# Optimization experiments

Hardware: AMD Instinct MI355X
Metric: run time of the kernel (lower is better)

Reference implementation:

```python
import jax, jax.numpy as jnp
import numpy as np

B, N, E = 4, 20000, 320000          # batch, billboards, edges
F_NODE, F_AD = 16, 8                # raw feature dims
H, L, HEADS = 64, 2, 4              # hidden, message-passing layers, attn heads


def layer_norm(x, g, b, eps=1e-5):
    mu = x.mean(-1, keepdims=True)
    var = ((x - mu) ** 2).mean(-1, keepdims=True)
    return (x - mu) / jnp.sqrt(var + eps) * g + b


def setup_inputs() -> dict:
    key = jax.random.key(0)
    ks = jax.random.split(key, 16)
    s = lambda i, shape, sc: jax.random.normal(ks[i], shape, jnp.float32) * sc
    return {
        'graph_nodes': s(0, (B, N, F_NODE), 1.0),
        'current_ad': s(1, (B, F_AD), 1.0),
        'w_node': s(2, (F_NODE, H), 0.1), 'b_node': jnp.zeros((H,), jnp.float32),
        'msg_w': s(3, (L, 2 * H, H), 0.05), 'msg_b': jnp.zeros((L, H), jnp.float32),
        'upd_w': s(4, (L, 2 * H, H), 0.05), 'upd_b': jnp.zeros((L, H), jnp.float32),
        'w_ad': s(5, (F_AD, H), 0.1), 'b_ad': jnp.zeros((H,), jnp.float32),
        'wq': s(6, (H, H), 0.1), 'bq': jnp.zeros((H,), jnp.float32),
        'wk': s(7, (H, H), 0.1), 'bk': jnp.zeros((H,), jnp.float32),
        'wv': s(8, (H, H), 0.1), 'bv': jnp.zeros((H,), jnp.float32),
        'wo': s(9, (H, H), 0.1), 'bo': jnp.zeros((H,), jnp.float32),
        'ln_g': jnp.ones((H,), jnp.float32), 'ln_b': jnp.zeros((H,), jnp.float32),
        'policy_w': s(10, (H,), 0.1), 'policy_b': jnp.zeros((), jnp.float32),
        'graph_edge_links': jax.random.randint(ks[11], (B, 2, E), 0, N),
        'mask': jax.random.randint(ks[12], (B, N), 0, 2).astype(bool),
    }


def reference(graph_nodes, current_ad, w_node, b_node, msg_w, msg_b, upd_w, upd_b,
              w_ad, b_ad, wq, bq, wk, bk, wv, bv, wo, bo, ln_g, ln_b,
              policy_w, policy_b, graph_edge_links, mask):
    # ---- node encoder ----
    h = jax.nn.relu(graph_nodes @ w_node + b_node)          # [B,N,H]
    src = graph_edge_links[:, 0, :]                          # [B,E]
    dst = graph_edge_links[:, 1, :]                          # [B,E]
    gather = jax.vmap(lambda hh, ii: hh[ii])                 # per-batch edge gather
    scatter = jax.vmap(lambda m, d: jax.ops.segment_sum(m, d, num_segments=N))
    # ---- message passing: gather -> MLP message -> scatter-add -> residual update ----
    for l in range(L):
        edge_in = jnp.concatenate([gather(h, src), gather(h, dst)], axis=-1)  # [B,E,2H]
        msg = jax.nn.relu(edge_in @ msg_w[l] + msg_b[l])                       # [B,E,H]
        agg = scatter(msg, dst)                                                # [B,N,H]
        h = h + jax.nn.relu(jnp.concatenate([h, agg], axis=-1) @ upd_w[l] + upd_b[l])
    # ---- ad encoder + multi-head attention (query=ad, key/value=billboards) ----
    a = jax.nn.relu(current_ad @ w_ad + b_ad)                # [B,H]
    dh = H // HEADS
    q = (a @ wq + bq).reshape(B, HEADS, 1, dh)               # [B,h,1,d]
    k = (h @ wk + bk).reshape(B, N, HEADS, dh).transpose(0, 2, 1, 3)  # [B,h,N,d]
    v = (h @ wv + bv).reshape(B, N, HEADS, dh).transpose(0, 2, 1, 3)
    att = jax.nn.softmax(jnp.einsum('bhqd,bhkd->bhqk', q, k) / jnp.sqrt(jnp.float32(dh)), axis=-1)
    ctx = jnp.einsum('bhqk,bhkd->bhqd', att, v).reshape(B, H)
    g = layer_norm(a + ctx @ wo + bo, ln_g, ln_b)            # residual + LN, [B,H]
    # ---- masked policy logits over billboards ----
    logits = jnp.einsum('bnh,bh->bn', h, g) / jnp.sqrt(jnp.float32(H)) + h @ policy_w + policy_b
    return jnp.where(mask, logits, jnp.float32(-1e9))
```

## Files before the change

### kernel.cpp

```cpp
#include <hip/hip_runtime.h>
#include <hip/hip_bf16.h>
#include <math.h>

constexpr int B_ = 4;
constexpr int N_ = 20000;
constexpr int E_ = 320000;
constexpr int HEADS_ = 4;
constexpr int NCH = 64;
constexpr int CS = (N_ + NCH - 1) / NCH;
constexpr int NT_ = (B_ * N_) / 16;
constexpr int NWIN = 1250;
constexpr int HWIN = 625;
constexpr int WCAP = 512;
constexpr int TPAD = 16;

typedef __attribute__((ext_vector_type(8))) short short8;
typedef __attribute__((ext_vector_type(4))) float f32x4;

constexpr size_t SZ_TDB   = (size_t)B_ * N_ * 64 * 2;
constexpr size_t SZ_AGG   = (size_t)B_ * N_ * 64 * 4;
constexpr size_t SZ_EBUCK = (size_t)B_ * NWIN * WCAP * 4;
constexpr size_t SZ_EPAIR = (size_t)B_ * E_ * 4;
constexpr size_t OFF_TDB  = 0;
constexpr size_t OFF_AGG  = SZ_TDB;
constexpr size_t OFF_EBUCK= OFF_AGG + SZ_AGG;
constexpr size_t OFF_EPAIR= OFF_EBUCK + SZ_EBUCK;
constexpr size_t OFF_HB16 = OFF_EPAIR + SZ_EPAIR;
constexpr size_t OFF_AVEC = OFF_HB16 + SZ_TDB;
constexpr size_t OFF_Q    = OFF_AVEC + 1024;
constexpr size_t OFF_CTX  = OFF_Q + 1024;
constexpr size_t OFF_WCMB = OFF_CTX + 1024;
constexpr size_t OFF_FLAG = OFF_WCMB + 1024;
constexpr size_t OFF_PART = OFF_FLAG + 64;
constexpr size_t OFF_TAILS= OFF_PART + 1024 * 18 * 4 + 64;
constexpr size_t OFF_WBASE= OFF_TAILS + (size_t)B_ * NWIN * TPAD * 4;
constexpr size_t OFF_VB16 = OFF_WBASE + (size_t)B_ * NWIN * 4 + 64;

static __device__ __forceinline__ unsigned short f2bf(float f) {
    union { float f; unsigned u; } v; v.f = f;
    unsigned r = v.u + 0x7fffu + ((v.u >> 16) & 1u);
    return (unsigned short)(r >> 16);
}
static __device__ __forceinline__ float bf2f(unsigned short u) {
    union { unsigned u; float f; } v; v.u = (unsigned)u << 16;
    return v.f;
}

__global__ void k_maskdetect(const unsigned int* __restrict__ m, int* __restrict__ flag) {
    if (blockIdx.x == 0 && threadIdx.x == 0) {
        bool alli = true, allf = true;
        for (int i = 0; i < 256; ++i) {
            unsigned v = m[i];
            alli = alli && (v <= 1u);
            allf = allf && (v == 0u || v == 0x3f800000u);
        }
        *flag = alli ? 1 : (allf ? 2 : 0);
    }
}

__global__ __launch_bounds__(256) void k_embed_bucket(const float* __restrict__ gn,
                                                      const float* __restrict__ wnod,
                                                      const float* __restrict__ bias,
                                                      unsigned short* __restrict__ hb16,
                                                      const int* __restrict__ links,
                                                      int* __restrict__ tails,
                                                      unsigned* __restrict__ ebuck) {
    int i = blockIdx.x;
    int g = i >> 3, r = i & 7;
    if (g % 5 == 4) {
        int eb = (g / 5) * 8 + r;
        int lane = threadIdx.x & 63;
        float wc[16];
#pragma unroll
        for (int k = 0; k < 16; ++k) wc[k] = wnod[k * 64 + lane];
        float bb = bias[lane];
        int gw = eb * 4 + (threadIdx.x >> 6);
        for (int node = gw; node < B_ * N_; node += 1248 * 4) {
            const float* rr = gn + (size_t)node * 16;
            float a0 = 0.f, a1 = 0.f, a2 = 0.f, a3 = 0.f;
#pragma unroll
            for (int k = 0; k < 16; k += 4) {
                a0 = fmaf(rr[k + 0], wc[k + 0], a0);
                a1 = fmaf(rr[k + 1], wc[k + 1], a1);
                a2 = fmaf(rr[k + 2], wc[k + 2], a2);
                a3 = fmaf(rr[k + 3], wc[k + 3], a3);
            }
            float v = fmaxf(bb + ((a0 + a1) + (a2 + a3)), 0.f);
            hb16[(size_t)node * 64 + lane] = f2bf(v);
        }
    } else {
        int og = g - (g + 1) / 5;
        int b = r >> 1;
        int half = r & 1;
        int e0 = og * 512 + threadIdx.x;
        const int* lsrc = links + (size_t)b * 2 * E_;
#pragma unroll
        for (int ch = 0; ch < 2; ++ch) {
            int e = e0 + ch * 256;
            unsigned src = (unsigned)lsrc[e];
            unsigned dst = (unsigned)lsrc[E_ + e];
            int w = dst >> 4;
            if ((w >= HWIN) == (half == 1)) {
                int slot = atomicAdd(&tails[(b * NWIN + w) * TPAD], 1);
                if (slot < WCAP)
                    ebuck[(size_t)(b * NWIN + w) * WCAP + slot] = (dst << 16) | src;
            }
        }
    }
}

__global__ __launch_bounds__(1024) void k_scan_tails(const int* __restrict__ tails,
                                                     int* __restrict__ wbase) {
    __shared__ int wsum[16];
    __shared__ int sbase;
    int b = blockIdx.x, t = threadIdx.x;
    int lane = t & 63, wv = t >> 6;
    if (t == 0) sbase = 0;
    __syncthreads();
    for (int base = 0; base < NWIN; base += 1024) {
        int idx = base + t;
        int c = 0;
        if (idx < NWIN) { c = tails[(b * NWIN + idx) * TPAD]; if (c > WCAP) c = WCAP; }
        int x = c;
#pragma unroll
        for (int o = 1; o < 64; o <<= 1) {
            int y = __shfl_up(x, o);
            if (lane >= o) x += y;
        }
        if (lane == 63) wsum[wv] = x;
        __syncthreads();
        if (wv == 0) {
            int s = (lane < 16) ? wsum[lane] : 0;
#pragma unroll
            for (int o = 1; o < 16; o <<= 1) {
                int y = __shfl_up(s, o);
                if (lane >= o) s += y;
            }
            if (lane < 16) wsum[lane] = s;
        }
        __syncthreads();
        int wpre = (wv > 0) ? wsum[wv - 1] : 0;
        int incl = x + wpre + sbase;
        if (idx < NWIN) wbase[b * NWIN + idx] = incl - c;
        __syncthreads();
        if (t == 1023) sbase = incl;
        __syncthreads();
    }
}

__global__ __launch_bounds__(256) void k_sortwin(const unsigned* __restrict__ ebuck,
                                                 const int* __restrict__ tails,
                                                 const int* __restrict__ wbase,
                                                 unsigned* __restrict__ epair) {
    __shared__ int hist[16], hbase[16];
    __shared__ unsigned sbuf[WCAP];
    int i = blockIdx.x;
    int r = i & 7;
    int b = r >> 1;
    int w = (i >> 3) + HWIN * (r & 1);
    int cntw = tails[(b * NWIN + w) * TPAD];
    if (cntw > WCAP) cntw = WCAP;
    if (threadIdx.x < 16) hist[threadIdx.x] = 0;
    __syncthreads();
    const unsigned* src = ebuck + (size_t)(b * NWIN + w) * WCAP;
    int idx0 = threadIdx.x, idx1 = threadIdx.x + 256;
    bool v0 = idx0 < cntw, v1 = idx1 < cntw;
    unsigned e0 = 0, e1 = 0;
    if (v0) { e0 = src[idx0]; atomicAdd(&hist[(e0 >> 16) & 15], 1); }
    if (v1) { e1 = src[idx1]; atomicAdd(&hist[(e1 >> 16) & 15], 1); }
    __syncthreads();
    if (threadIdx.x == 0) {
        int run = 0;
#pragma unroll
        for (int p = 0; p < 16; ++p) { hbase[p] = run; run += hist[p]; }
    }
    __syncthreads();
    if (threadIdx.x < 16) hist[threadIdx.x] = 0;
    __syncthreads();
    if (v0) { int bn = (e0 >> 16) & 15; sbuf[hbase[bn] + atomicAdd(&hist[bn], 1)] = e0; }
    if (v1) { int bn = (e1 >> 16) & 15; sbuf[hbase[bn] + atomicAdd(&hist[bn], 1)] = e1; }
    __syncthreads();
    int gb = wbase[b * NWIN + w];
    unsigned* dst = epair + (size_t)b * E_ + gb;
    for (int idx = threadIdx.x; idx < cntw; idx += 256) dst[idx] = sbuf[idx];
}

__global__ __launch_bounds__(256) void k_tdst_mfma(const unsigned short* __restrict__ hb16,
                                                   const float* __restrict__ mw,
                                                   const float* __restrict__ mb,
                                                   unsigned short* __restrict__ tdb) {
    int lane = threadIdx.x & 63;
    int g = lane >> 4, c = lane & 15;
    short8 bf[4][2];
#pragma unroll
    for (int nt = 0; nt < 4; ++nt)
#pragma unroll
        for (int ks = 0; ks < 2; ++ks)
#pragma unroll
            for (int j = 0; j < 8; ++j)
                bf[nt][ks][j] = (short)f2bf(mw[(64 + ks * 32 + g * 8 + j) * 64 + nt * 16 + c]);
    float mbv[4];
#pragma unroll
    for (int nt = 0; nt < 4; ++nt) mbv[nt] = mb[nt * 16 + c];

    int wid = blockIdx.x * 4 + (threadIdx.x >> 6);
    int nw = gridDim.x * 4;
    f32x4 zero = {0.f, 0.f, 0.f, 0.f};
    for (int t = wid; t < NT_; t += nw) {
        const unsigned short* ap = hb16 + ((size_t)t * 16 + c) * 64;
        short8 a0 = *(const short8*)(ap + g * 8);
        short8 a1 = *(const short8*)(ap + 32 + g * 8);
        f32x4 acc[4];
#pragma unroll
        for (int nt = 0; nt < 4; ++nt) {
            acc[nt] = __builtin_amdgcn_mfma_f32_16x16x32_bf16(a0, bf[nt][0], zero, 0, 0, 0);
            acc[nt] = __builtin_amdgcn_mfma_f32_16x16x32_bf16(a1, bf[nt][1], acc[nt], 0, 0, 0);
        }
#pragma unroll
        for (int r = 0; r < 4; ++r) {
            size_t row = (size_t)t * 16 + 4 * g + r;
            unsigned long long pk =
                (unsigned long long)f2bf(acc[0][r] + mbv[0])
              | ((unsigned long long)f2bf(acc[1][r] + mbv[1]) << 16)
              | ((unsigned long long)f2bf(acc[2][r] + mbv[2]) << 32)
              | ((unsigned long long)f2bf(acc[3][r] + mbv[3]) << 48);
            *(unsigned long long*)(tdb + row * 64 + c * 4) = pk;
        }
    }
}

__global__ __launch_bounds__(256) void k_edge_mfma(const unsigned short* __restrict__ hb16,
                                                   const unsigned short* __restrict__ tdb,
                                                   const unsigned* __restrict__ epair,
                                                   const float* __restrict__ mw,
                                                   float* __restrict__ agg) {
    int lane = threadIdx.x & 63;
    int g = lane >> 4, c = lane & 15;
    short8 bf[4][2];
#pragma unroll
    for (int nt = 0; nt < 4; ++nt)
#pragma unroll
        for (int ks = 0; ks < 2; ++ks)
#pragma unroll
            for (int j = 0; j < 8; ++j)
                bf[nt][ks][j] = (short)f2bf(mw[(ks * 32 + g * 8 + j) * 64 + nt * 16 + c]);

    int i = blockIdx.x;
    int b = (i & 7) >> 1;
    int o = ((i >> 3) << 1) | (i & 1);
    int w = threadIdx.x >> 6;
    const unsigned* pp = epair + (size_t)b * E_;
    const unsigned short* hbase = hb16 + (size_t)(b * N_) * 64;
    const unsigned short* tbase = tdb + (size_t)(b * N_) * 64;
    float* abase = agg + (size_t)(b * N_) * 64;

    bool hi1 = (lane & 32) != 0;
    bool hi0 = (lane & 16) != 0;

    unsigned pr[4];
#pragma unroll
    for (int k = 0; k < 4; ++k) {
        int t0 = (o * 4 + w) + k * 5000;
        pr[k] = pp[t0 * 16 + c];
    }
    short8 a0[4], a1[4];
#pragma unroll
    for (int k = 0; k < 4; ++k) {
        const unsigned short* hrow = hbase + (size_t)(pr[k] & 0xFFFFu) * 64;
        a0[k] = *(const short8*)(hrow + g * 8);
        a1[k] = *(const short8*)(hrow + 32 + g * 8);
    }

    f32x4 zero = {0.f, 0.f, 0.f, 0.f};
#pragma unroll
    for (int k = 0; k < 4; ++k) {
        int dval = (int)(pr[k] >> 16);
        f32x4 acc[4];
#pragma unroll
        for (int nt = 0; nt < 4; ++nt) {
            acc[nt] = __builtin_amdgcn_mfma_f32_16x16x32_bf16(a0[k], bf[nt][0], zero, 0, 0, 0);
            acc[nt] = __builtin_amdgcn_mfma_f32_16x16x32_bf16(a1[k], bf[nt][1], acc[nt], 0, 0, 0);
        }

        float val[4][4];
#pragma unroll
        for (int r = 0; r < 4; ++r) {
            int dr = __shfl(dval, 4 * g + r);
            unsigned long long tv = *(const unsigned long long*)(tbase + (size_t)dr * 64 + c * 4);
            val[0][r] = fmaxf(acc[0][r] + bf2f((unsigned short)(tv       & 0xFFFFu)), 0.f);
            val[1][r] = fmaxf(acc[1][r] + bf2f((unsigned short)((tv >> 16) & 0xFFFFu)), 0.f);
            val[2][r] = fmaxf(acc[2][r] + bf2f((unsigned short)((tv >> 32) & 0xFFFFu)), 0.f);
            val[3][r] = fmaxf(acc[3][r] + bf2f((unsigned short)((tv >> 48) & 0xFFFFu)), 0.f);
        }

        int prev = __shfl(dval, (lane + 63) & 63);
        bool head = (c == 0) || (dval != prev);
        unsigned long long bal = __ballot(head);
        unsigned m16 = (unsigned)(bal & 0xFFFFu);

        while (m16) {
            int ii = __ffs(m16) - 1;
            unsigned rest = m16 & (m16 - 1);
            int jj = rest ? (__ffs(rest) - 1) : 16;
            m16 = rest;
            int d = __shfl(dval, ii);

            float v0 = 0.f, v1 = 0.f, v2 = 0.f, v3 = 0.f;
#pragma unroll
            for (int r = 0; r < 4; ++r) {
                int rr = 4 * g + r;
                bool in = (rr >= ii) && (rr < jj);
                v0 += in ? val[0][r] : 0.f;
                v1 += in ? val[1][r] : 0.f;
                v2 += in ? val[2][r] : 0.f;
                v3 += in ? val[3][r] : 0.f;
            }
            float sA0 = hi1 ? v0 : v2;
            float sA1 = hi1 ? v1 : v3;
            float rA0 = __shfl_xor(sA0, 32);
            float rA1 = __shfl_xor(sA1, 32);
            float w0 = (hi1 ? v2 : v0) + rA0;
            float w1 = (hi1 ? v3 : v1) + rA1;
            float sB = hi0 ? w0 : w1;
            float rB = __shfl_xor(sB, 16);
            float outv = (hi0 ? w1 : w0) + rB;

            atomicAdd(&abase[(size_t)d * 64 + lane], outv);
        }
    }
}

__global__ __launch_bounds__(256) void k_upd_tdst_mfma(unsigned short* __restrict__ hb16,
                                                       const float* __restrict__ agg,
                                                       const float* __restrict__ uw,
                                                       const float* __restrict__ ub,
                                                       const float* __restrict__ mw2,
                                                       const float* __restrict__ mb2,
                                                       unsigned short* __restrict__ tdb) {
    __shared__ unsigned short stile[4][1024];
    int lane = threadIdx.x & 63;
    int g = lane >> 4, c = lane & 15;
    int wv = threadIdx.x >> 6;
    short8 bh[4][2], ba[4][2], bt[4][2];
#pragma unroll
    for (int nt = 0; nt < 4; ++nt)
#pragma unroll
        for (int ks = 0; ks < 2; ++ks)
#pragma unroll
            for (int j = 0; j < 8; ++j) {
                bh[nt][ks][j] = (short)f2bf(uw[(ks * 32 + g * 8 + j) * 64 + nt * 16 + c]);
                ba[nt][ks][j] = (short)f2bf(uw[(64 + ks * 32 + g * 8 + j) * 64 + nt * 16 + c]);
                bt[nt][ks][j] = (short)f2bf(mw2[(64 + ks * 32 + g * 8 + j) * 64 + nt * 16 + c]);
            }
    float ubv[4], mbv[4];
#pragma unroll
    for (int nt = 0; nt < 4; ++nt) { ubv[nt] = ub[nt * 16 + c]; mbv[nt] = mb2[nt * 16 + c]; }

    int wid = blockIdx.x * 4 + wv;
    int nw = gridDim.x * 4;
    f32x4 zero = {0.f, 0.f, 0.f, 0.f};
    int xr = (c & 7) << 3;
    for (int t = wid; t < NT_; t += nw) {
        unsigned short* ap = hb16 + ((size_t)t * 16 + c) * 64;
        short8 a0 = *(const short8*)(ap + g * 8);
        short8 a1 = *(const short8*)(ap + 32 + g * 8);

        const float* gp = agg + ((size_t)t * 16 + c) * 64;
        float4 q0 = *(const float4*)(gp + g * 8);
        float4 q1 = *(const float4*)(gp + g * 8 + 4);
        float4 q2 = *(const float4*)(gp + 32 + g * 8);
        float4 q3 = *(const float4*)(gp + 32 + g * 8 + 4);
        short8 s0, s1;
        s0[0] = (short)f2bf(q0.x); s0[1] = (short)f2bf(q0.y);
        s0[2] = (short)f2bf(q0.z); s0[3] = (short)f2bf(q0.w);
        s0[4] = (short)f2bf(q1.x); s0[5] = (short)f2bf(q1.y);
        s0[6] = (short)f2bf(q1.z); s0[7] = (short)f2bf(q1.w);
        s1[0] = (short)f2bf(q2.x); s1[1] = (short)f2bf(q2.y);
        s1[2] = (short)f2bf(q2.z); s1[3] = (short)f2bf(q2.w);
        s1[4] = (short)f2bf(q3.x); s1[5] = (short)f2bf(q3.y);
        s1[6] = (short)f2bf(q3.z); s1[7] = (short)f2bf(q3.w);

        f32x4 acc[4];
#pragma unroll
        for (int nt = 0; nt < 4; ++nt) {
            acc[nt] = __builtin_amdgcn_mfma_f32_16x16x32_bf16(a0, bh[nt][0], zero, 0, 0, 0);
            acc[nt] = __builtin_amdgcn_mfma_f32_16x16x32_bf16(a1, bh[nt][1], acc[nt], 0, 0, 0);
            acc[nt] = __builtin_amdgcn_mfma_f32_16x16x32_bf16(s0, ba[nt][0], acc[nt], 0, 0, 0);
            acc[nt] = __builtin_amdgcn_mfma_f32_16x16x32_bf16(s1, ba[nt][1], acc[nt], 0, 0, 0);
        }
#pragma unroll
        for (int r = 0; r < 4; ++r) {
            size_t row = (size_t)t * 16 + 4 * g + r;
            int lrow = 4 * g + r;
#pragma unroll
            for (int nt = 0; nt < 4; ++nt) {
                size_t idx = row * 64 + nt * 16 + c;
                float v = bf2f(hb16[idx]) + fmaxf(acc[nt][r] + ubv[nt], 0.f);
                unsigned short vb = f2bf(v);
                hb16[idx] = vb;
                int col = nt * 16 + c;
                stile[wv][lrow * 64 + (col ^ ((lrow & 7) << 3))] = vb;
            }
        }
        short8 na0 = *(const short8*)&stile[wv][c * 64 + ((g * 8) ^ xr)];
        short8 na1 = *(const short8*)&stile[wv][c * 64 + ((32 + g * 8) ^ xr)];
        f32x4 tacc[4];
#pragma unroll
        for (int nt = 0; nt < 4; ++nt) {
            tacc[nt] = __builtin_amdgcn_mfma_f32_16x16x32_bf16(na0, bt[nt][0], zero, 0, 0, 0);
            tacc[nt] = __builtin_amdgcn_mfma_f32_16x16x32_bf16(na1, bt[nt][1], tacc[nt], 0, 0, 0);
        }
#pragma unroll
        for (int r = 0; r < 4; ++r) {
            size_t row = (size_t)t * 16 + 4 * g + r;
            unsigned long long pk =
                (unsigned long long)f2bf(tacc[0][r] + mbv[0])
              | ((unsigned long long)f2bf(tacc[1][r] + mbv[1]) << 16)
              | ((unsigned long long)f2bf(tacc[2][r] + mbv[2]) << 32)
              | ((unsigned long long)f2bf(tacc[3][r] + mbv[3]) << 48);
            *(unsigned long long*)(tdb + row * 64 + c * 4) = pk;
        }
    }
}

__global__ __launch_bounds__(256) void k_upd_kv_mfma(unsigned short* __restrict__ hb16,
                                                     const float* __restrict__ agg,
                                                     const float* __restrict__ uw,
                                                     const float* __restrict__ ub,
                                                     const float* __restrict__ wk,
                                                     const float* __restrict__ bk,
                                                     const float* __restrict__ wv,
                                                     const float* __restrict__ bv,
                                                     unsigned short* __restrict__ kb16,
                                                     unsigned short* __restrict__ vb16) {
    __shared__ unsigned short stile[4][1024];
    int lane = threadIdx.x & 63;
    int g = lane >> 4, c = lane & 15;
    int wvv = threadIdx.x >> 6;
    short8 bh[4][2], ba[4][2], bkf[4][2], bvf[4][2];
#pragma unroll
    for (int nt = 0; nt < 4; ++nt)
#pragma unroll
        for (int ks = 0; ks < 2; ++ks)
#pragma unroll
            for (int j = 0; j < 8; ++j) {
                bh[nt][ks][j]  = (short)f2bf(uw[(ks * 32 + g * 8 + j) * 64 + nt * 16 + c]);
                ba[nt][ks][j]  = (short)f2bf(uw[(64 + ks * 32 + g * 8 + j) * 64 + nt * 16 + c]);
                bkf[nt][ks][j] = (short)f2bf(wk[(ks * 32 + g * 8 + j) * 64 + nt * 16 + c]);
                bvf[nt][ks][j] = (short)f2bf(wv[(ks * 32 + g * 8 + j) * 64 + nt * 16 + c]);
            }
    float ubv[4], bkv[4], bvv[4];
#pragma unroll
    for (int nt = 0; nt < 4; ++nt) {
        ubv[nt] = ub[nt * 16 + c];
        bkv[nt] = bk[nt * 16 + c];
        bvv[nt] = bv[nt * 16 + c];
    }

    int wid = blockIdx.x * 4 + wvv;
    int nw = gridDim.x * 4;
    f32x4 zero = {0.f, 0.f, 0.f, 0.f};
    int xr = (c & 7) << 3;
    for (int t = wid; t < NT_; t += nw) {
        unsigned short* ap = hb16 + ((size_t)t * 16 + c) * 64;
        short8 a0 = *(const short8*)(ap + g * 8);
        short8 a1 = *(const short8*)(ap + 32 + g * 8);

        const float* gp = agg + ((size_t)t * 16 + c) * 64;
        float4 q0 = *(const float4*)(gp + g * 8);
        float4 q1 = *(const float4*)(gp + g * 8 + 4);
        float4 q2 = *(const float4*)(gp + 32 + g * 8);
        float4 q3 = *(const float4*)(gp + 32 + g * 8 + 4);
        short8 s0, s1;
        s0[0] = (short)f2bf(q0.x); s0[1] = (short)f2bf(q0.y);
        s0[2] = (short)f2bf(q0.z); s0[3] = (short)f2bf(q0.w);
        s0[4] = (short)f2bf(q1.x); s0[5] = (short)f2bf(q1.y);
        s0[6] = (short)f2bf(q1.z); s0[7] = (short)f2bf(q1.w);
        s1[0] = (short)f2bf(q2.x); s1[1] = (short)f2bf(q2.y);
        s1[2] = (short)f2bf(q2.z); s1[3] = (short)f2bf(q2.w);
        s1[4] = (short)f2bf(q3.x); s1[5] = (short)f2bf(q3.y);
        s1[6] = (short)f2bf(q3.z); s1[7] = (short)f2bf(q3.w);

        f32x4 acc[4];
#pragma unroll
        for (int nt = 0; nt < 4; ++nt) {
            acc[nt] = __builtin_amdgcn_mfma_f32_16x16x32_bf16(a0, bh[nt][0], zero, 0, 0, 0);
            acc[nt] = __builtin_amdgcn_mfma_f32_16x16x32_bf16(a1, bh[nt][1], acc[nt], 0, 0, 0);
            acc[nt] = __builtin_amdgcn_mfma_f32_16x16x32_bf16(s0, ba[nt][0], acc[nt], 0, 0, 0);
            acc[nt] = __builtin_amdgcn_mfma_f32_16x16x32_bf16(s1, ba[nt][1], acc[nt], 0, 0, 0);
        }
#pragma unroll
        for (int r = 0; r < 4; ++r) {
            size_t row = (size_t)t * 16 + 4 * g + r;
            int lrow = 4 * g + r;
#pragma unroll
            for (int nt = 0; nt < 4; ++nt) {
                size_t idx = row * 64 + nt * 16 + c;
                float v = bf2f(hb16[idx]) + fmaxf(acc[nt][r] + ubv[nt], 0.f);
                unsigned short vb = f2bf(v);
                hb16[idx] = vb;
                int col = nt * 16 + c;
                stile[wvv][lrow * 64 + (col ^ ((lrow & 7) << 3))] = vb;
            }
        }
        short8 na0 = *(const short8*)&stile[wvv][c * 64 + ((g * 8) ^ xr)];
        short8 na1 = *(const short8*)&stile[wvv][c * 64 + ((32 + g * 8) ^ xr)];
        f32x4 ak[4], av[4];
#pragma unroll
        for (int nt = 0; nt < 4; ++nt) {
            ak[nt] = __builtin_amdgcn_mfma_f32_16x16x32_bf16(na0, bkf[nt][0], zero, 0, 0, 0);
            ak[nt] = __builtin_amdgcn_mfma_f32_16x16x32_bf16(na1, bkf[nt][1], ak[nt], 0, 0, 0);
            av[nt] = __builtin_amdgcn_mfma_f32_16x16x32_bf16(na0, bvf[nt][0], zero, 0, 0, 0);
            av[nt] = __builtin_amdgcn_mfma_f32_16x16x32_bf16(na1, bvf[nt][1], av[nt], 0, 0, 0);
        }
#pragma unroll
        for (int r = 0; r < 4; ++r) {
            size_t row = (size_t)t * 16 + 4 * g + r;
#pragma unroll
            for (int nt = 0; nt < 4; ++nt) {
                kb16[row * 64 + nt * 16 + c] = f2bf(ak[nt][r] + bkv[nt]);
                vb16[row * 64 + nt * 16 + c] = f2bf(av[nt][r] + bvv[nt]);
            }
        }
    }
}

__global__ __launch_bounds__(64) void k_aq(const float* __restrict__ ad,
                                           const float* __restrict__ wad,
                                           const float* __restrict__ bad,
                                           const float* __restrict__ wq,
                                           const float* __restrict__ bq,
                                           float* __restrict__ a_out,
                                           float* __restrict__ q_out) {
    int b = blockIdx.x, t = threadIdx.x;
    __shared__ float sa[64];
    float acc = bad[t];
#pragma unroll
    for (int i = 0; i < 8; ++i) acc = fmaf(ad[b * 8 + i], wad[i * 64 + t], acc);
    float av = fmaxf(acc, 0.f);
    sa[t] = av;
    a_out[b * 64 + t] = av;
    __syncthreads();
    float qa = bq[t];
    for (int i = 0; i < 64; ++i) qa = fmaf(sa[i], wq[i * 64 + t], qa);
    q_out[b * 64 + t] = qa;
}

__global__ __launch_bounds__(256) void k_attn(const float* __restrict__ q,
                                              const unsigned short* __restrict__ kb16,
                                              const unsigned short* __restrict__ vb16,
                                              float* __restrict__ part) {
    int id = blockIdx.x;
    int ch = id % NCH;
    int bh = id / NCH;
    int b = bh / HEADS_, hd = bh % HEADS_;
    float qv[16];
#pragma unroll
    for (int d = 0; d < 16; ++d) qv[d] = q[b * 64 + hd * 16 + d];
    float m = -1e30f, s = 0.f, c[16];
#pragma unroll
    for (int d = 0; d < 16; ++d) c[d] = 0.f;
    int n0 = ch * CS;
    int n1 = n0 + CS; if (n1 > N_) n1 = N_;
    for (int n = n0 + threadIdx.x; n < n1; n += 256) {
        const short8* kr = (const short8*)(kb16 + ((size_t)b * N_ + n) * 64 + hd * 16);
        short8 k0 = kr[0], k1 = kr[1];
        float dot = 0.f;
#pragma unroll
        for (int d = 0; d < 8; ++d) {
            dot = fmaf(qv[d], bf2f((unsigned short)k0[d]), dot);
            dot = fmaf(qv[8 + d], bf2f((unsigned short)k1[d]), dot);
        }
        dot *= 0.25f;
        float nm = fmaxf(m, dot);
        float p = __expf(dot - nm);
        float cor = __expf(m - nm);
        const short8* vr = (const short8*)(vb16 + ((size_t)b * N_ + n) * 64 + hd * 16);
        short8 v0 = vr[0], v1 = vr[1];
        s = s * cor + p;
#pragma unroll
        for (int d = 0; d < 8; ++d) {
            c[d] = c[d] * cor + p * bf2f((unsigned short)v0[d]);
            c[8 + d] = c[8 + d] * cor + p * bf2f((unsigned short)v1[d]);
        }
        m = nm;
    }
#pragma unroll
    for (int o = 1; o < 64; o <<= 1) {
        float m2 = __shfl_xor(m, o);
        float s2 = __shfl_xor(s, o);
        float nm = fmaxf(m, m2);
        float w1 = __expf(m - nm), w2 = __expf(m2 - nm);
        s = s * w1 + s2 * w2;
#pragma unroll
        for (int d = 0; d < 16; ++d) {
            float c2 = __shfl_xor(c[d], o);
            c[d] = c[d] * w1 + c2 * w2;
        }
        m = nm;
    }
    __shared__ float red[4][18];
    int wv_ = threadIdx.x >> 6, lane = threadIdx.x & 63;
    if (lane == 0) {
        red[wv_][0] = m; red[wv_][1] = s;
#pragma unroll
        for (int d = 0; d < 16; ++d) red[wv_][2 + d] = c[d];
    }
    __syncthreads();
    if (threadIdx.x == 0) {
        float gm = red[0][0];
        for (int w = 1; w < 4; ++w) gm = fmaxf(gm, red[w][0]);
        float gs = 0.f, gc[16];
#pragma unroll
        for (int d = 0; d < 16; ++d) gc[d] = 0.f;
        for (int w = 0; w < 4; ++w) {
            float ww = __expf(red[w][0] - gm);
            gs += red[w][1] * ww;
#pragma unroll
            for (int d = 0; d < 16; ++d) gc[d] += red[w][2 + d] * ww;
        }
        float* p = part + (size_t)id * 18;
        p[0] = gm; p[1] = gs;
#pragma unroll
        for (int d = 0; d < 16; ++d) p[2 + d] = gc[d];
    }
}

__global__ __launch_bounds__(64) void k_comb(const float* __restrict__ part,
                                             float* __restrict__ ctx) {
    int bh = blockIdx.x, t = threadIdx.x;
    int b = bh / HEADS_, hd = bh % HEADS_;
    const float* p = part + ((size_t)bh * NCH + t) * 18;
    float m = p[0], s = p[1], c[16];
#pragma unroll
    for (int d = 0; d < 16; ++d) c[d] = p[2 + d];
    float gm = m;
#pragma unroll
    for (int o = 1; o < 64; o <<= 1) gm = fmaxf(gm, __shfl_xor(gm, o));
    float w = __expf(m - gm);
    float sw = s * w;
#pragma unroll
    for (int o = 1; o < 64; o <<= 1) sw += __shfl_xor(sw, o);
    float cg[16];
#pragma unroll
    for (int d = 0; d < 16; ++d) {
        float x = c[d] * w;
#pragma unroll
        for (int o = 1; o < 64; o <<= 1) x += __shfl_xor(x, o);
        cg[d] = x;
    }
    if (t == 0) {
#pragma unroll
        for (int d = 0; d < 16; ++d) ctx[b * 64 + hd * 16 + d] = cg[d] / sw;
    }
}

__global__ __launch_bounds__(64) void k_g(const float* __restrict__ a,
                                          const float* __restrict__ ctx,
                                          const float* __restrict__ wo,
                                          const float* __restrict__ bo,
                                          const float* __restrict__ lng,
                                          const float* __restrict__ lnb,
                                          const float* __restrict__ pw,
                                          float* __restrict__ wcomb) {
    int b = blockIdx.x, t = threadIdx.x;
    __shared__ float sc[64];
    sc[t] = ctx[b * 64 + t];
    __syncthreads();
    float o = bo[t];
    for (int i = 0; i < 64; ++i) o = fmaf(sc[i], wo[i * 64 + t], o);
    float y = a[b * 64 + t] + o;
    float mu = y;
#pragma unroll
    for (int oo = 1; oo < 64; oo <<= 1) mu += __shfl_xor(mu, oo);
    mu *= (1.f / 64.f);
    float d = y - mu;
    float var = d * d;
#pragma unroll
    for (int oo = 1; oo < 64; oo <<= 1) var += __shfl_xor(var, oo);
    var *= (1.f / 64.f);
    float g = d * rsqrtf(var + 1e-5f) * lng[t] + lnb[t];
    wcomb[b * 64 + t] = g * 0.125f + pw[t];
}

__global__ __launch_bounds__(256) void k_final(const unsigned short* __restrict__ hb16,
                                               const float* __restrict__ wcomb,
                                               const float* __restrict__ pb,
                                               const void* __restrict__ mask,
                                               const int* __restrict__ flagp,
                                               float* __restrict__ out) {
    int idx = blockIdx.x * 256 + threadIdx.x;
    if (idx >= B_ * N_) return;
    int b = idx / N_;
    const float* wr = wcomb + b * 64;
    const short8* hr = (const short8*)(hb16 + (size_t)idx * 64);
    float acc = pb[0];
#pragma unroll
    for (int i = 0; i < 8; ++i) {
        short8 hv = hr[i];
#pragma unroll
        for (int j = 0; j < 8; ++j)
            acc = fmaf(bf2f((unsigned short)hv[j]), wr[i * 8 + j], acc);
    }
    int flag = *flagp;
    bool mv;
    if (flag == 1)      mv = ((const int*)mask)[idx] != 0;
    else if (flag == 2) mv = ((const float*)mask)[idx] != 0.f;
    else                mv = ((const unsigned char*)mask)[idx] != 0;
    out[idx] = mv ? acc : -1.0e9f;
}

extern "C" void kernel_launch(void* const* d_in, const int* in_sizes, int n_in,
                              void* d_out, int out_size, void* d_ws, size_t ws_size,
                              hipStream_t stream) {
    const float* gn   = (const float*)d_in[0];
    const float* ad   = (const float*)d_in[1];
    const float* wnod = (const float*)d_in[2];
    const float* bnod = (const float*)d_in[3];
    const float* msgw = (const float*)d_in[4];
    const float* msgb = (const float*)d_in[5];
    const float* updw = (const float*)d_in[6];
    const float* updb = (const float*)d_in[7];
    const float* wad  = (const float*)d_in[8];
    const float* bad  = (const float*)d_in[9];
    const float* wq   = (const float*)d_in[10];
    const float* bq   = (const float*)d_in[11];
    const float* wk   = (const float*)d_in[12];
    const float* bk   = (const float*)d_in[13];
    const float* wv   = (const float*)d_in[14];
    const float* bv   = (const float*)d_in[15];
    const float* wo   = (const float*)d_in[16];
    const float* bo   = (const float*)d_in[17];
    const float* lng  = (const float*)d_in[18];
    const float* lnb  = (const float*)d_in[19];
    const float* pw   = (const float*)d_in[20];
    const float* pb   = (const float*)d_in[21];
    const int*   links= (const int*)d_in[22];
    const void*  mask = d_in[23];

    char* ws = (char*)d_ws;
    unsigned short* tdb  = (unsigned short*)(ws + OFF_TDB);
    unsigned short* kb16 = (unsigned short*)(ws + OFF_TDB);
    float* agg  = (float*)(ws + OFF_AGG);
    unsigned* ebuck = (unsigned*)(ws + OFF_EBUCK);
    unsigned* epair = (unsigned*)(ws + OFF_EPAIR);
    unsigned short* hb16 = (unsigned short*)(ws + OFF_HB16);
    float* avec = (float*)(ws + OFF_AVEC);
    float* qvec = (float*)(ws + OFF_Q);
    float* ctx  = (float*)(ws + OFF_CTX);
    float* wcmb = (float*)(ws + OFF_WCMB);
    int*   flag = (int*)(ws + OFF_FLAG);
    float* part = (float*)(ws + OFF_PART);
    int*   tails= (int*)(ws + OFF_TAILS);
    int*   wbase= (int*)(ws + OFF_WBASE);
    unsigned short* vb16 = (unsigned short*)(ws + OFF_VB16);
    float* out  = (float*)d_out;

    hipMemsetAsync(tails, 0, (size_t)B_ * NWIN * TPAD * 4, stream);
    k_maskdetect<<<1, 1, 0, stream>>>((const unsigned int*)mask, flag);
    k_embed_bucket<<<6248, 256, 0, stream>>>(gn, wnod, bnod, hb16, links, tails, ebuck);
    k_scan_tails<<<B_, 1024, 0, stream>>>(tails, wbase);
    k_sortwin<<<5000, 256, 0, stream>>>(ebuck, tails, wbase, epair);

    k_tdst_mfma<<<512, 256, 0, stream>>>(hb16, msgw, msgb, tdb);
    hipMemsetAsync(agg, 0, SZ_AGG, stream);
    k_edge_mfma<<<5000, 256, 0, stream>>>(hb16, tdb, epair, msgw, agg);
    k_upd_tdst_mfma<<<512, 256, 0, stream>>>(hb16, agg, updw, updb,
                                             msgw + (size_t)128 * 64, msgb + 64, tdb);
    hipMemsetAsync(agg, 0, SZ_AGG, stream);
    k_edge_mfma<<<5000, 256, 0, stream>>>(hb16, tdb, epair, msgw + (size_t)128 * 64, agg);
    k_upd_kv_mfma<<<512, 256, 0, stream>>>(hb16, agg, updw + (size_t)128 * 64, updb + 64,
                                           wk, bk, wv, bv, kb16, vb16);

    k_aq<<<B_, 64, 0, stream>>>(ad, wad, bad, wq, bq, avec, qvec);
    k_attn<<<B_ * HEADS_ * NCH, 256, 0, stream>>>(qvec, kb16, vb16, part);
    k_comb<<<B_ * HEADS_, 64, 0, stream>>>(part, ctx);
    k_g<<<B_, 64, 0, stream>>>(avec, ctx, wo, bo, lng, lnb, pw, wcmb);
    k_final<<<(B_ * N_ + 255) / 256, 256, 0, stream>>>(hb16, wcmb, pb, mask, flag, out);
}
```

Before: 257.1 us.

## Fold agg zeroing into producer kernels and process 32-edge tiles per wave

The two full-size memsets of the aggregation buffer are removed. The buffer is now zeroed inside the kernels that already touch it: the first-layer projection kernel, and the update kernel right after it reads agg for the next layer. The edge kernel now handles two 16-edge MFMA tiles together, preloads the destination-term bias as the MFMA accumulator, and runs one segmented reduction over 32 sorted edges. That should cut the number of per-destination atomic adds and raise load-level parallelism, at the cost of more registers per thread.

```diff
diff --git a/kernel.cpp b/kernel.cpp
--- a/kernel.cpp
+++ b/kernel.cpp
@@ -188,7 +188,8 @@
 __global__ __launch_bounds__(256) void k_tdst_mfma(const unsigned short* __restrict__ hb16,
                                                    const float* __restrict__ mw,
                                                    const float* __restrict__ mb,
-                                                   unsigned short* __restrict__ tdb) {
+                                                   unsigned short* __restrict__ tdb,
+                                                   float* __restrict__ agg) {
     int lane = threadIdx.x & 63;
     int g = lane >> 4, c = lane & 15;
     short8 bf[4][2];
@@ -225,6 +226,7 @@
               | ((unsigned long long)f2bf(acc[2][r] + mbv[2]) << 32)
               | ((unsigned long long)f2bf(acc[3][r] + mbv[3]) << 48);
             *(unsigned long long*)(tdb + row * 64 + c * 4) = pk;
+            *(f32x4*)(agg + row * 64 + c * 4) = zero;
         }
     }
 }
@@ -257,63 +259,93 @@
     bool hi1 = (lane & 32) != 0;
     bool hi0 = (lane & 16) != 0;
 
-    unsigned pr[4];
-#pragma unroll
-    for (int k = 0; k < 4; ++k) {
-        int t0 = (o * 4 + w) + k * 5000;
-        pr[k] = pp[t0 * 16 + c];
-    }
-    short8 a0[4], a1[4];
-#pragma unroll
-    for (int k = 0; k < 4; ++k) {
-        const unsigned short* hrow = hbase + (size_t)(pr[k] & 0xFFFFu) * 64;
-        a0[k] = *(const short8*)(hrow + g * 8);
-        a1[k] = *(const short8*)(hrow + 32 + g * 8);
-    }
-
-    f32x4 zero = {0.f, 0.f, 0.f, 0.f};
-#pragma unroll
-    for (int k = 0; k < 4; ++k) {
-        int dval = (int)(pr[k] >> 16);
-        f32x4 acc[4];
+    unsigned prA[2], prB[2];
+#pragma unroll
+    for (int k = 0; k < 2; ++k) {
+        int s0 = ((o * 4 + w) + k * 5000) * 32;
+        prA[k] = pp[s0 + c];
+        prB[k] = pp[s0 + 16 + c];
+    }
+    short8 a0A[2], a1A[2], a0B[2], a1B[2];
+#pragma unroll
+    for (int k = 0; k < 2; ++k) {
+        const unsigned short* hrA = hbase + (size_t)(prA[k] & 0xFFFFu) * 64;
+        a0A[k] = *(const short8*)(hrA + g * 8);
+        a1A[k] = *(const short8*)(hrA + 32 + g * 8);
+        const unsigned short* hrB = hbase + (size_t)(prB[k] & 0xFFFFu) * 64;
+        a0B[k] = *(const short8*)(hrB + g * 8);
+        a1B[k] = *(const short8*)(hrB + 32 + g * 8);
+    }
+
+#pragma unroll
+    for (int k = 0; k < 2; ++k) {
+        int dA = (int)(prA[k] >> 16);
+        int dB = (int)(prB[k] >> 16);
+
+        unsigned long long tvA[4], tvB[4];
+#pragma unroll
+        for (int r = 0; r < 4; ++r) {
+            int drA = __shfl(dA, 4 * g + r);
+            tvA[r] = *(const unsigned long long*)(tbase + (size_t)drA * 64 + c * 4);
+            int drB = __shfl(dB, 4 * g + r);
+            tvB[r] = *(const unsigned long long*)(tbase + (size_t)drB * 64 + c * 4);
+        }
+        f32x4 accA[4], accB[4];
 #pragma unroll
         for (int nt = 0; nt < 4; ++nt) {
-            acc[nt] = __builtin_amdgcn_mfma_f32_16x16x32_bf16(a0[k], bf[nt][0], zero, 0, 0, 0);
-            acc[nt] = __builtin_amdgcn_mfma_f32_16x16x32_bf16(a1[k], bf[nt][1], acc[nt], 0, 0, 0);
-        }
-
-        float val[4][4];
-#pragma unroll
-        for (int r = 0; r < 4; ++r) {
-            int dr = __shfl(dval, 4 * g + r);
-            unsigned long long tv = *(const unsigned long long*)(tbase + (size_t)dr * 64 + c * 4);
-            val[0][r] = fmaxf(acc[0][r] + bf2f((unsigned short)(tv       & 0xFFFFu)), 0.f);
-            val[1][r] = fmaxf(acc[1][r] + bf2f((unsigned short)((tv >> 16) & 0xFFFFu)), 0.f);
-            val[2][r] = fmaxf(acc[2][r] + bf2f((unsigned short)((tv >> 32) & 0xFFFFu)), 0.f);
-            val[3][r] = fmaxf(acc[3][r] + bf2f((unsigned short)((tv >> 48) & 0xFFFFu)), 0.f);
-        }
-
-        int prev = __shfl(dval, (lane + 63) & 63);
-        bool head = (c == 0) || (dval != prev);
-        unsigned long long bal = __ballot(head);
-        unsigned m16 = (unsigned)(bal & 0xFFFFu);
-
-        while (m16) {
-            int ii = __ffs(m16) - 1;
-            unsigned rest = m16 & (m16 - 1);
-            int jj = rest ? (__ffs(rest) - 1) : 16;
-            m16 = rest;
-            int d = __shfl(dval, ii);
+#pragma unroll
+            for (int r = 0; r < 4; ++r) {
+                accA[nt][r] = bf2f((unsigned short)((tvA[r] >> (16 * nt)) & 0xFFFFu));
+                accB[nt][r] = bf2f((unsigned short)((tvB[r] >> (16 * nt)) & 0xFFFFu));
+            }
+        }
+#pragma unroll
+        for (int nt = 0; nt < 4; ++nt) {
+            accA[nt] = __builtin_amdgcn_mfma_f32_16x16x32_bf16(a0A[k], bf[nt][0], accA[nt], 0, 0, 0);
+            accA[nt] = __builtin_amdgcn_mfma_f32_16x16x32_bf16(a1A[k], bf[nt][1], accA[nt], 0, 0, 0);
+            accB[nt] = __builtin_amdgcn_mfma_f32_16x16x32_bf16(a0B[k], bf[nt][0], accB[nt], 0, 0, 0);
+            accB[nt] = __builtin_amdgcn_mfma_f32_16x16x32_bf16(a1B[k], bf[nt][1], accB[nt], 0, 0, 0);
+        }
+        float valA[4][4], valB[4][4];
+#pragma unroll
+        for (int nt = 0; nt < 4; ++nt)
+#pragma unroll
+            for (int r = 0; r < 4; ++r) {
+                valA[nt][r] = fmaxf(accA[nt][r], 0.f);
+                valB[nt][r] = fmaxf(accB[nt][r], 0.f);
+            }
+
+        int prevA = __shfl(dA, (lane + 63) & 63);
+        bool headA = (c == 0) || (dA != prevA);
+        int lastA = __shfl(dA, 15);
+        int prevB = __shfl(dB, (lane + 63) & 63);
+        bool headB = (c == 0) ? (dB != lastA) : (dB != prevB);
+        unsigned long long balA = __ballot(headA);
+        unsigned long long balB = __ballot(headB);
+        unsigned m32 = (unsigned)(balA & 0xFFFFu) | ((unsigned)(balB & 0xFFFFu) << 16);
+
+        while (m32) {
+            int ii = __ffs(m32) - 1;
+            unsigned rest = m32 & (m32 - 1);
+            int jj = rest ? (__ffs(rest) - 1) : 32;
+            m32 = rest;
+            int d = (ii < 16) ? __shfl(dA, ii) : __shfl(dB, ii - 16);
 
             float v0 = 0.f, v1 = 0.f, v2 = 0.f, v3 = 0.f;
 #pragma unroll
             for (int r = 0; r < 4; ++r) {
-                int rr = 4 * g + r;
-                bool in = (rr >= ii) && (rr < jj);
-                v0 += in ? val[0][r] : 0.f;
-                v1 += in ? val[1][r] : 0.f;
-                v2 += in ? val[2][r] : 0.f;
-                v3 += in ? val[3][r] : 0.f;
+                int rrA = 4 * g + r;
+                bool inA = (rrA >= ii) && (rrA < jj);
+                v0 += inA ? valA[0][r] : 0.f;
+                v1 += inA ? valA[1][r] : 0.f;
+                v2 += inA ? valA[2][r] : 0.f;
+                v3 += inA ? valA[3][r] : 0.f;
+                int rrB = 16 + 4 * g + r;
+                bool inB = (rrB >= ii) && (rrB < jj);
+                v0 += inB ? valB[0][r] : 0.f;
+                v1 += inB ? valB[1][r] : 0.f;
+                v2 += inB ? valB[2][r] : 0.f;
+                v3 += inB ? valB[3][r] : 0.f;
             }
             float sA0 = hi1 ? v0 : v2;
             float sA1 = hi1 ? v1 : v3;
@@ -331,7 +363,7 @@
 }
 
 __global__ __launch_bounds__(256) void k_upd_tdst_mfma(unsigned short* __restrict__ hb16,
-                                                       const float* __restrict__ agg,
+                                                       float* __restrict__ agg,
                                                        const float* __restrict__ uw,
                                                        const float* __restrict__ ub,
                                                        const float* __restrict__ mw2,
@@ -365,11 +397,15 @@
         short8 a0 = *(const short8*)(ap + g * 8);
         short8 a1 = *(const short8*)(ap + 32 + g * 8);
 
-        const float* gp = agg + ((size_t)t * 16 + c) * 64;
+        float* gp = agg + ((size_t)t * 16 + c) * 64;
         float4 q0 = *(const float4*)(gp + g * 8);
         float4 q1 = *(const float4*)(gp + g * 8 + 4);
         float4 q2 = *(const float4*)(gp + 32 + g * 8);
         float4 q3 = *(const float4*)(gp + 32 + g * 8 + 4);
+        *(f32x4*)(gp + g * 8) = zero;
+        *(f32x4*)(gp + g * 8 + 4) = zero;
+        *(f32x4*)(gp + 32 + g * 8) = zero;
+        *(f32x4*)(gp + 32 + g * 8 + 4) = zero;
         short8 s0, s1;
         s0[0] = (short)f2bf(q0.x); s0[1] = (short)f2bf(q0.y);
         s0[2] = (short)f2bf(q0.z); s0[3] = (short)f2bf(q0.w);
@@ -762,12 +798,10 @@
     k_scan_tails<<<B_, 1024, 0, stream>>>(tails, wbase);
     k_sortwin<<<5000, 256, 0, stream>>>(ebuck, tails, wbase, epair);
 
-    k_tdst_mfma<<<512, 256, 0, stream>>>(hb16, msgw, msgb, tdb);
-    hipMemsetAsync(agg, 0, SZ_AGG, stream);
+    k_tdst_mfma<<<512, 256, 0, stream>>>(hb16, msgw, msgb, tdb, agg);
     k_edge_mfma<<<5000, 256, 0, stream>>>(hb16, tdb, epair, msgw, agg);
     k_upd_tdst_mfma<<<512, 256, 0, stream>>>(hb16, agg, updw, updb,
                                              msgw + (size_t)128 * 64, msgb + 64, tdb);
-    hipMemsetAsync(agg, 0, SZ_AGG, stream);
     k_edge_mfma<<<5000, 256, 0, stream>>>(hb16, tdb, epair, msgw + (size_t)128 * 64, agg);
     k_upd_kv_mfma<<<512, 256, 0, stream>>>(hb16, agg, updw + (size_t)128 * 64, updb + 64,
                                            wk, bk, wv, bv, kb16, vb16);
```

New measurement: 254.6 us. No clear change (-1.0%).

## Fuse window sort into edge kernel with shared-memory aggregation per destination window

Applied to the files above, without the earlier changes.

Drops the scan and sort kernels and the global edge-pair array. Each edge block now sorts its destination window's bucket in shared memory, runs the message MFMA with the dst term preloaded into the accumulator, and accumulates into a shared 16x64 tile. It then writes that tile to agg with plain stores, so the agg memsets and the global atomics go away. In exchange each block's work depends on its window's edge count, so load may be uneven, and the sort is repeated in both layers.

```diff
diff --git a/kernel.cpp b/kernel.cpp
--- a/kernel.cpp
+++ b/kernel.cpp
@@ -20,12 +20,10 @@
 constexpr size_t SZ_TDB   = (size_t)B_ * N_ * 64 * 2;
 constexpr size_t SZ_AGG   = (size_t)B_ * N_ * 64 * 4;
 constexpr size_t SZ_EBUCK = (size_t)B_ * NWIN * WCAP * 4;
-constexpr size_t SZ_EPAIR = (size_t)B_ * E_ * 4;
 constexpr size_t OFF_TDB  = 0;
 constexpr size_t OFF_AGG  = SZ_TDB;
 constexpr size_t OFF_EBUCK= OFF_AGG + SZ_AGG;
-constexpr size_t OFF_EPAIR= OFF_EBUCK + SZ_EBUCK;
-constexpr size_t OFF_HB16 = OFF_EPAIR + SZ_EPAIR;
+constexpr size_t OFF_HB16 = OFF_EBUCK + SZ_EBUCK;
 constexpr size_t OFF_AVEC = OFF_HB16 + SZ_TDB;
 constexpr size_t OFF_Q    = OFF_AVEC + 1024;
 constexpr size_t OFF_CTX  = OFF_Q + 1024;
@@ -33,8 +31,7 @@
 constexpr size_t OFF_FLAG = OFF_WCMB + 1024;
 constexpr size_t OFF_PART = OFF_FLAG + 64;
 constexpr size_t OFF_TAILS= OFF_PART + 1024 * 18 * 4 + 64;
-constexpr size_t OFF_WBASE= OFF_TAILS + (size_t)B_ * NWIN * TPAD * 4;
-constexpr size_t OFF_VB16 = OFF_WBASE + (size_t)B_ * NWIN * 4 + 64;
+constexpr size_t OFF_VB16 = OFF_TAILS + (size_t)B_ * NWIN * TPAD * 4;
 
 static __device__ __forceinline__ unsigned short f2bf(float f) {
     union { float f; unsigned u; } v; v.f = f;
@@ -109,82 +106,6 @@
     }
 }
 
-__global__ __launch_bounds__(1024) void k_scan_tails(const int* __restrict__ tails,
-                                                     int* __restrict__ wbase) {
-    __shared__ int wsum[16];
-    __shared__ int sbase;
-    int b = blockIdx.x, t = threadIdx.x;
-    int lane = t & 63, wv = t >> 6;
-    if (t == 0) sbase = 0;
-    __syncthreads();
-    for (int base = 0; base < NWIN; base += 1024) {
-        int idx = base + t;
-        int c = 0;
-        if (idx < NWIN) { c = tails[(b * NWIN + idx) * TPAD]; if (c > WCAP) c = WCAP; }
-        int x = c;
-#pragma unroll
-        for (int o = 1; o < 64; o <<= 1) {
-            int y = __shfl_up(x, o);
-            if (lane >= o) x += y;
-        }
-        if (lane == 63) wsum[wv] = x;
-        __syncthreads();
-        if (wv == 0) {
-            int s = (lane < 16) ? wsum[lane] : 0;
-#pragma unroll
-            for (int o = 1; o < 16; o <<= 1) {
-                int y = __shfl_up(s, o);
-                if (lane >= o) s += y;
-            }
-            if (lane < 16) wsum[lane] = s;
-        }
-        __syncthreads();
-        int wpre = (wv > 0) ? wsum[wv - 1] : 0;
-        int incl = x + wpre + sbase;
-        if (idx < NWIN) wbase[b * NWIN + idx] = incl - c;
-        __syncthreads();
-        if (t == 1023) sbase = incl;
-        __syncthreads();
-    }
-}
-
-__global__ __launch_bounds__(256) void k_sortwin(const unsigned* __restrict__ ebuck,
-                                                 const int* __restrict__ tails,
-                                                 const int* __restrict__ wbase,
-                                                 unsigned* __restrict__ epair) {
-    __shared__ int hist[16], hbase[16];
-    __shared__ unsigned sbuf[WCAP];
-    int i = blockIdx.x;
-    int r = i & 7;
-    int b = r >> 1;
-    int w = (i >> 3) + HWIN * (r & 1);
-    int cntw = tails[(b * NWIN + w) * TPAD];
-    if (cntw > WCAP) cntw = WCAP;
-    if (threadIdx.x < 16) hist[threadIdx.x] = 0;
-    __syncthreads();
-    const unsigned* src = ebuck + (size_t)(b * NWIN + w) * WCAP;
-    int idx0 = threadIdx.x, idx1 = threadIdx.x + 256;
-    bool v0 = idx0 < cntw, v1 = idx1 < cntw;
-    unsigned e0 = 0, e1 = 0;
-    if (v0) { e0 = src[idx0]; atomicAdd(&hist[(e0 >> 16) & 15], 1); }
-    if (v1) { e1 = src[idx1]; atomicAdd(&hist[(e1 >> 16) & 15], 1); }
-    __syncthreads();
-    if (threadIdx.x == 0) {
-        int run = 0;
-#pragma unroll
-        for (int p = 0; p < 16; ++p) { hbase[p] = run; run += hist[p]; }
-    }
-    __syncthreads();
-    if (threadIdx.x < 16) hist[threadIdx.x] = 0;
-    __syncthreads();
-    if (v0) { int bn = (e0 >> 16) & 15; sbuf[hbase[bn] + atomicAdd(&hist[bn], 1)] = e0; }
-    if (v1) { int bn = (e1 >> 16) & 15; sbuf[hbase[bn] + atomicAdd(&hist[bn], 1)] = e1; }
-    __syncthreads();
-    int gb = wbase[b * NWIN + w];
-    unsigned* dst = epair + (size_t)b * E_ + gb;
-    for (int idx = threadIdx.x; idx < cntw; idx += 256) dst[idx] = sbuf[idx];
-}
-
 __global__ __launch_bounds__(256) void k_tdst_mfma(const unsigned short* __restrict__ hb16,
                                                    const float* __restrict__ mw,
                                                    const float* __restrict__ mb,
@@ -229,13 +150,24 @@
     }
 }
 
-__global__ __launch_bounds__(256) void k_edge_mfma(const unsigned short* __restrict__ hb16,
-                                                   const unsigned short* __restrict__ tdb,
-                                                   const unsigned* __restrict__ epair,
-                                                   const float* __restrict__ mw,
-                                                   float* __restrict__ agg) {
+__global__ __launch_bounds__(256) void k_edge_win(const unsigned short* __restrict__ hb16,
+                                                  const unsigned short* __restrict__ tdb,
+                                                  const unsigned* __restrict__ ebuck,
+                                                  const int* __restrict__ tails,
+                                                  const float* __restrict__ mw,
+                                                  float* __restrict__ agg) {
+    __shared__ int hist[16], hbase[16];
+    __shared__ unsigned sbuf[WCAP];
+    __shared__ float lacc[16 * 64];
+    int i = blockIdx.x;
+    int r8 = i & 7;
+    int b = r8 >> 1;
+    int w = (i >> 3) + HWIN * (r8 & 1);
+    int n0 = w * 16;
     int lane = threadIdx.x & 63;
     int g = lane >> 4, c = lane & 15;
+    int wv = threadIdx.x >> 6;
+
     short8 bf[4][2];
 #pragma unroll
     for (int nt = 0; nt < 4; ++nt)
@@ -245,52 +177,71 @@
             for (int j = 0; j < 8; ++j)
                 bf[nt][ks][j] = (short)f2bf(mw[(ks * 32 + g * 8 + j) * 64 + nt * 16 + c]);
 
-    int i = blockIdx.x;
-    int b = (i & 7) >> 1;
-    int o = ((i >> 3) << 1) | (i & 1);
-    int w = threadIdx.x >> 6;
-    const unsigned* pp = epair + (size_t)b * E_;
-    const unsigned short* hbase = hb16 + (size_t)(b * N_) * 64;
+    int cnt = tails[(b * NWIN + w) * TPAD];
+    if (cnt > WCAP) cnt = WCAP;
+
+    f32x4 zero = {0.f, 0.f, 0.f, 0.f};
+    ((f32x4*)lacc)[threadIdx.x] = zero;
+    if (threadIdx.x < 16) hist[threadIdx.x] = 0;
+    __syncthreads();
+
+    const unsigned* src = ebuck + (size_t)(b * NWIN + w) * WCAP;
+    int idx0 = threadIdx.x, idx1 = threadIdx.x + 256;
+    bool v0 = idx0 < cnt, v1 = idx1 < cnt;
+    unsigned e0 = 0, e1 = 0;
+    if (v0) { e0 = src[idx0]; atomicAdd(&hist[(e0 >> 16) & 15], 1); }
+    if (v1) { e1 = src[idx1]; atomicAdd(&hist[(e1 >> 16) & 15], 1); }
+    __syncthreads();
+    if (threadIdx.x == 0) {
+        int run = 0;
+#pragma unroll
+        for (int p = 0; p < 16; ++p) { hbase[p] = run; run += hist[p]; }
+    }
+    __syncthreads();
+    if (threadIdx.x < 16) hist[threadIdx.x] = 0;
+    __syncthreads();
+    if (v0) { int bn = (e0 >> 16) & 15; sbuf[hbase[bn] + atomicAdd(&hist[bn], 1)] = e0; }
+    if (v1) { int bn = (e1 >> 16) & 15; sbuf[hbase[bn] + atomicAdd(&hist[bn], 1)] = e1; }
+    __syncthreads();
+
+    const unsigned short* hb = hb16 + (size_t)(b * N_) * 64;
     const unsigned short* tbase = tdb + (size_t)(b * N_) * 64;
-    float* abase = agg + (size_t)(b * N_) * 64;
-
     bool hi1 = (lane & 32) != 0;
     bool hi0 = (lane & 16) != 0;
-
-    unsigned pr[4];
-#pragma unroll
-    for (int k = 0; k < 4; ++k) {
-        int t0 = (o * 4 + w) + k * 5000;
-        pr[k] = pp[t0 * 16 + c];
-    }
-    short8 a0[4], a1[4];
-#pragma unroll
-    for (int k = 0; k < 4; ++k) {
-        const unsigned short* hrow = hbase + (size_t)(pr[k] & 0xFFFFu) * 64;
-        a0[k] = *(const short8*)(hrow + g * 8);
-        a1[k] = *(const short8*)(hrow + 32 + g * 8);
-    }
-
-    f32x4 zero = {0.f, 0.f, 0.f, 0.f};
-#pragma unroll
-    for (int k = 0; k < 4; ++k) {
-        int dval = (int)(pr[k] >> 16);
-        f32x4 acc[4];
-#pragma unroll
-        for (int nt = 0; nt < 4; ++nt) {
-            acc[nt] = __builtin_amdgcn_mfma_f32_16x16x32_bf16(a0[k], bf[nt][0], zero, 0, 0, 0);
-            acc[nt] = __builtin_amdgcn_mfma_f32_16x16x32_bf16(a1[k], bf[nt][1], acc[nt], 0, 0, 0);
-        }
-
-        float val[4][4];
+    unsigned padv = (unsigned)n0 << 16;
+
+    for (int s0 = wv * 16; s0 < cnt; s0 += 64) {
+        int sl = s0 + c;
+        unsigned pr = (sl < cnt) ? sbuf[sl] : padv;
+        int dval = (int)(pr >> 16);
+        const unsigned short* hrow = hb + (size_t)(pr & 0xFFFFu) * 64;
+        short8 a0 = *(const short8*)(hrow + g * 8);
+        short8 a1 = *(const short8*)(hrow + 32 + g * 8);
+
+        unsigned long long tv[4];
 #pragma unroll
         for (int r = 0; r < 4; ++r) {
             int dr = __shfl(dval, 4 * g + r);
-            unsigned long long tv = *(const unsigned long long*)(tbase + (size_t)dr * 64 + c * 4);
-            val[0][r] = fmaxf(acc[0][r] + bf2f((unsigned short)(tv       & 0xFFFFu)), 0.f);
-            val[1][r] = fmaxf(acc[1][r] + bf2f((unsigned short)((tv >> 16) & 0xFFFFu)), 0.f);
-            val[2][r] = fmaxf(acc[2][r] + bf2f((unsigned short)((tv >> 32) & 0xFFFFu)), 0.f);
-            val[3][r] = fmaxf(acc[3][r] + bf2f((unsigned short)((tv >> 48) & 0xFFFFu)), 0.f);
+            tv[r] = *(const unsigned long long*)(tbase + (size_t)dr * 64 + c * 4);
+        }
+        f32x4 acc[4];
+#pragma unroll
+        for (int nt = 0; nt < 4; ++nt)
+#pragma unroll
+            for (int r = 0; r < 4; ++r)
+                acc[nt][r] = bf2f((unsigned short)((tv[r] >> (16 * nt)) & 0xFFFFu));
+#pragma unroll
+        for (int nt = 0; nt < 4; ++nt) {
+            acc[nt] = __builtin_amdgcn_mfma_f32_16x16x32_bf16(a0, bf[nt][0], acc[nt], 0, 0, 0);
+            acc[nt] = __builtin_amdgcn_mfma_f32_16x16x32_bf16(a1, bf[nt][1], acc[nt], 0, 0, 0);
+        }
+        float val[4][4];
+#pragma unroll
+        for (int r = 0; r < 4; ++r) {
+            bool okr = (s0 + 4 * g + r) < cnt;
+#pragma unroll
+            for (int nt = 0; nt < 4; ++nt)
+                val[nt][r] = okr ? fmaxf(acc[nt][r], 0.f) : 0.f;
         }
 
         int prev = __shfl(dval, (lane + 63) & 63);
@@ -305,29 +256,33 @@
             m16 = rest;
             int d = __shfl(dval, ii);
 
-            float v0 = 0.f, v1 = 0.f, v2 = 0.f, v3 = 0.f;
+            float v0s = 0.f, v1s = 0.f, v2s = 0.f, v3s = 0.f;
 #pragma unroll
             for (int r = 0; r < 4; ++r) {
                 int rr = 4 * g + r;
                 bool in = (rr >= ii) && (rr < jj);
-                v0 += in ? val[0][r] : 0.f;
-                v1 += in ? val[1][r] : 0.f;
-                v2 += in ? val[2][r] : 0.f;
-                v3 += in ? val[3][r] : 0.f;
+                v0s += in ? val[0][r] : 0.f;
+                v1s += in ? val[1][r] : 0.f;
+                v2s += in ? val[2][r] : 0.f;
+                v3s += in ? val[3][r] : 0.f;
             }
-            float sA0 = hi1 ? v0 : v2;
-            float sA1 = hi1 ? v1 : v3;
+            float sA0 = hi1 ? v0s : v2s;
+            float sA1 = hi1 ? v1s : v3s;
             float rA0 = __shfl_xor(sA0, 32);
             float rA1 = __shfl_xor(sA1, 32);
-            float w0 = (hi1 ? v2 : v0) + rA0;
-            float w1 = (hi1 ? v3 : v1) + rA1;
+            float w0 = (hi1 ? v2s : v0s) + rA0;
+            float w1 = (hi1 ? v3s : v1s) + rA1;
             float sB = hi0 ? w0 : w1;
             float rB = __shfl_xor(sB, 16);
             float outv = (hi0 ? w1 : w0) + rB;
 
-            atomicAdd(&abase[(size_t)d * 64 + lane], outv);
-        }
-    }
+            atomicAdd(&lacc[(d - n0) * 64 + lane], outv);
+        }
+    }
+    __syncthreads();
+
+    f32x4* ab = (f32x4*)(agg + ((size_t)(b * N_) + n0) * 64);
+    ab[threadIdx.x] = ((const f32x4*)lacc)[threadIdx.x];
 }
 
 __global__ __launch_bounds__(256) void k_upd_tdst_mfma(unsigned short* __restrict__ hb16,
@@ -743,7 +698,6 @@
     unsigned short* kb16 = (unsigned short*)(ws + OFF_TDB);
     float* agg  = (float*)(ws + OFF_AGG);
     unsigned* ebuck = (unsigned*)(ws + OFF_EBUCK);
-    unsigned* epair = (unsigned*)(ws + OFF_EPAIR);
     unsigned short* hb16 = (unsigned short*)(ws + OFF_HB16);
     float* avec = (float*)(ws + OFF_AVEC);
     float* qvec = (float*)(ws + OFF_Q);
@@ -752,23 +706,19 @@
     int*   flag = (int*)(ws + OFF_FLAG);
     float* part = (float*)(ws + OFF_PART);
     int*   tails= (int*)(ws + OFF_TAILS);
-    int*   wbase= (int*)(ws + OFF_WBASE);
     unsigned short* vb16 = (unsigned short*)(ws + OFF_VB16);
     float* out  = (float*)d_out;
 
     hipMemsetAsync(tails, 0, (size_t)B_ * NWIN * TPAD * 4, stream);
     k_maskdetect<<<1, 1, 0, stream>>>((const unsigned int*)mask, flag);
     k_embed_bucket<<<6248, 256, 0, stream>>>(gn, wnod, bnod, hb16, links, tails, ebuck);
-    k_scan_tails<<<B_, 1024, 0, stream>>>(tails, wbase);
-    k_sortwin<<<5000, 256, 0, stream>>>(ebuck, tails, wbase, epair);
 
     k_tdst_mfma<<<512, 256, 0, stream>>>(hb16, msgw, msgb, tdb);
-    hipMemsetAsync(agg, 0, SZ_AGG, stream);
-    k_edge_mfma<<<5000, 256, 0, stream>>>(hb16, tdb, epair, msgw, agg);
+    k_edge_win<<<5000, 256, 0, stream>>>(hb16, tdb, ebuck, tails, msgw, agg);
     k_upd_tdst_mfma<<<512, 256, 0, stream>>>(hb16, agg, updw, updb,
                                              msgw + (size_t)128 * 64, msgb + 64, tdb);
-    hipMemsetAsync(agg, 0, SZ_AGG, stream);
-    k_edge_mfma<<<5000, 256, 0, stream>>>(hb16, tdb, epair, msgw + (size_t)128 * 64, agg);
+    k_edge_win<<<5000, 256, 0, stream>>>(hb16, tdb, ebuck, tails,
+                                         msgw + (size_t)128 * 64, agg);
     k_upd_kv_mfma<<<512, 256, 0, stream>>>(hb16, agg, updw + (size_t)128 * 64, updb + 64,
                                            wk, bk, wv, bv, kb16, vb16);
 
```

After: 294.6 us. 1.15x slower.
